# Kernel optimization log

Hardware: AMD Instinct MI355X
Metric: run time of the kernel (lower is better)

## Reference

```python
import jax, jax.numpy as jnp
import numpy as np

PASSES = 6
S = 2           # numEdgeSets
D = 256         # inputLayerSize
OUT = 10        # outputLayerSize
HID = 80
B, N, E = 4, 10000, 160000


def _leaky(x):
    return jax.nn.leaky_relu(x, negative_slope=0.01)


def setup_inputs() -> dict:
    key = jax.random.key(0)
    ks = jax.random.split(key, 18)
    sc = 0.05
    return {
        "nodes": jax.random.normal(ks[0], (B, N, D), jnp.float32),
        "edges": jax.random.randint(ks[1], (B, S, E, 2), 0, N, jnp.int32),
        "problem_type": jax.random.uniform(ks[2], (B, 1), jnp.float32),
        # GRUCell params (torch layout: [3D, D] for ih and hh)
        "gru_w_ih": jax.random.normal(ks[3], (3 * D, D), jnp.float32) * sc,
        "gru_w_hh": jax.random.normal(ks[4], (3 * D, D), jnp.float32) * sc,
        "gru_b_ih": jax.random.normal(ks[5], (3 * D,), jnp.float32) * sc,
        "gru_b_hh": jax.random.normal(ks[6], (3 * D,), jnp.float32) * sc,
        # per-edge-set 2-layer MLP, stacked over edge sets
        "edge_w1": jax.random.normal(ks[7], (S, D, D), jnp.float32) * sc,
        "edge_b1": jax.random.normal(ks[8], (S, D), jnp.float32) * sc,
        "edge_w2": jax.random.normal(ks[9], (S, D, D), jnp.float32) * sc,
        "edge_b2": jax.random.normal(ks[10], (S, D), jnp.float32) * sc,
        # readout head
        "fc1_w": jax.random.normal(ks[11], (HID, D + 1), jnp.float32) * sc,
        "fc1_b": jax.random.normal(ks[12], (HID,), jnp.float32) * sc,
        "fc2_w": jax.random.normal(ks[13], (HID, HID), jnp.float32) * sc,
        "fc2_b": jax.random.normal(ks[14], (HID,), jnp.float32) * sc,
        "fc3_w": jax.random.normal(ks[15], (OUT, HID), jnp.float32) * sc,
        "fc3_b": jax.random.normal(ks[16], (OUT,), jnp.float32) * sc,
    }


def _gru_cell(x, h, w_ih, w_hh, b_ih, b_hh):
    # torch.nn.GRUCell semantics; x,h: [B,N,D]
    gi = jnp.einsum("bnd,ed->bne", x, w_ih) + b_ih   # [B,N,3D]
    gh = jnp.einsum("bnd,ed->bne", h, w_hh) + b_hh
    i_r, i_z, i_n = jnp.split(gi, 3, axis=-1)
    h_r, h_z, h_n = jnp.split(gh, 3, axis=-1)
    r = jax.nn.sigmoid(i_r + h_r)
    z = jax.nn.sigmoid(i_z + h_z)
    n = jnp.tanh(i_n + r * h_n)
    return (1.0 - z) * n + z * h


def reference(nodes, edges, problem_type, gru_w_ih, gru_w_hh, gru_b_ih, gru_b_hh,
              edge_w1, edge_b1, edge_w2, edge_b2,
              fc1_w, fc1_b, fc2_w, fc2_b, fc3_w, fc3_b):
    bidx = jnp.arange(B)[:, None]  # [B,1] for batched scatter
    h = nodes
    for j in range(PASSES):
        incoming = jnp.zeros_like(h)
        for si in range(S):
            dst = edges[:, si, :, 0]  # [B,E]
            src = edges[:, si, :, 1]  # [B,E]
            gathered = jnp.take_along_axis(h, src[:, :, None], axis=1)  # [B,E,D]
            y = _leaky(jnp.einsum("bed,fd->bef", gathered, edge_w1[si]) + edge_b1[si])
            y = jnp.einsum("bed,fd->bef", y, edge_w2[si]) + edge_b2[si]
            incoming = incoming.at[bidx, dst].add(y)
        h = _gru_cell(incoming, h, gru_w_ih, gru_w_hh, gru_b_ih, gru_b_hh)
        if j < PASSES - 2:
            h = jax.lax.stop_gradient(h)  # mirrors .detach()
    # graph readout: sum over nodes, log, nan->0, relu, +inf->finite max
    s = jnp.sum(h, axis=1)               # [B,D]
    l = jnp.log(s)
    l = jnp.where(jnp.isnan(l), 0.0, l)
    l = jax.nn.relu(l)
    finite_max = jnp.max(jnp.where(jnp.isinf(l), -jnp.inf, l), axis=1, keepdims=True)
    l = jnp.where(jnp.isinf(l), finite_max, l)
    x = jnp.concatenate([l, problem_type], axis=1)  # [B,D+1]
    x = _leaky(x @ fc1_w.T + fc1_b)
    x = _leaky(x @ fc2_w.T + fc2_b)
    return x @ fc3_w.T + fc3_b  # [B,OUT]
```

## Files before the change

### kernel.cpp

```cpp
#include <hip/hip_runtime.h>
#include <math.h>

#define NNODES 10000
#define NEDGES 160000
#define DIM    256
#define BATCH  4
#define NG     8
#define MROWS  40064
#define RBLK128 313
#define RGRP128 40

typedef __attribute__((ext_vector_type(8))) __bf16 bf16x8;
typedef __attribute__((ext_vector_type(4))) float  floatx4;
typedef __attribute__((ext_vector_type(8))) unsigned short ushort8v;

__device__ __forceinline__ float leakyf(float x){ return x > 0.f ? x : 0.01f*x; }
__device__ __forceinline__ float fsig(float x){ return 1.f/(1.f + __expf(-x)); }
__device__ __forceinline__ float ftanh(float x){ return 1.f - 2.f/(1.f + __expf(2.f*x)); }
__device__ __forceinline__ unsigned short f2bf_u(float x){
  unsigned int u = __float_as_uint(x);
  u += 0x7fffu + ((u >> 16) & 1u);
  return (unsigned short)(u >> 16);
}
__device__ __forceinline__ float bfdec(unsigned short u){
  return __uint_as_float(((unsigned int)u) << 16);
}
#define GATE_SCL 65535.f
#define GATE_INV 1.5259021896696422e-5f

#define VMCNT8 asm volatile("s_waitcnt vmcnt(8)" ::: "memory")
#define VMCNT4 asm volatile("s_waitcnt vmcnt(4)" ::: "memory")
#define VMCNT0 asm volatile("s_waitcnt vmcnt(0)" ::: "memory")
#define LGKM0  asm volatile("s_waitcnt lgkmcnt(0)" ::: "memory")
#define SBAR   __builtin_amdgcn_s_barrier()
#define SCHEDB __builtin_amdgcn_sched_barrier(0)
#define PRIO1  __builtin_amdgcn_s_setprio(1)
#define PRIO0  __builtin_amdgcn_s_setprio(0)

__device__ __forceinline__ void glds16(unsigned short* lds, const unsigned short* g){
  __builtin_amdgcn_global_load_lds(
      (const __attribute__((address_space(1))) void*)g,
      (__attribute__((address_space(3))) void*)lds, 16, 0, 0);
}

__device__ __forceinline__ ushort8v gload16(const unsigned short* p){
  ushort8v r;
  asm volatile("global_load_dwordx4 %0, %1, off" : "=&v"(r) : "v"(p));
  return r;
}

__global__ void ihinit_kernel(const float* __restrict__ nodes,
                              unsigned short* __restrict__ ihcat,
                              unsigned short* __restrict__ h_lo){
  int idx = blockIdx.x*256 + threadIdx.x;
  int base = idx*4;
  int row = base >> 8, d = base & 255;
  float4 v = *(const float4*)&nodes[base];
  unsigned short h0=f2bf_u(v.x), h1=f2bf_u(v.y), h2=f2bf_u(v.z), h3=f2bf_u(v.w);
  ushort4 hi; hi.x=h0; hi.y=h1; hi.z=h2; hi.w=h3;
  *(ushort4*)&ihcat[(size_t)row*512 + 256 + d] = hi;
  ushort4 lo;
  lo.x = f2bf_u(v.x - bfdec(h0));
  lo.y = f2bf_u(v.y - bfdec(h1));
  lo.z = f2bf_u(v.z - bfdec(h2));
  lo.w = f2bf_u(v.w - bfdec(h3));
  *(ushort4*)&h_lo[base] = lo;
}

__global__ void w1cat_kernel(const float* __restrict__ ew1, unsigned short* __restrict__ o){
  int idx = blockIdx.x*256 + threadIdx.x;
  int n = idx >> 8, k = idx & 255;
  o[idx] = f2bf_u(ew1[(n>>8)*65536 + (n&255)*256 + k]);
}
__global__ void w2k_kernel(const float* __restrict__ ew2, unsigned short* __restrict__ o){
  int idx = blockIdx.x*256 + threadIdx.x;
  int n = idx >> 10, kp = idx & 1023;
  int j = kp & 511, term = kp >> 9;
  int si = j >> 8, k = j & 255;
  float v = ew2[si*65536 + n*256 + k];
  unsigned short h = f2bf_u(v);
  o[idx] = term ? f2bf_u(v - bfdec(h)) : h;
}
__global__ void wk2_kernel(const float* __restrict__ w, unsigned short* __restrict__ o){
  int idx = blockIdx.x*256 + threadIdx.x;
  int c = idx >> 9, kp = idx & 511;
  int k = kp & 255, term = kp >> 8;
  float v = w[c*256 + k];
  unsigned short h = f2bf_u(v);
  o[idx] = term ? f2bf_u(v - bfdec(h)) : h;
}
__global__ void wcomb_kernel(const float* __restrict__ wih, const float* __restrict__ whh,
                             unsigned short* __restrict__ o){
  int idx = blockIdx.x*256 + threadIdx.x;
  int c = idx >> 10, kp = idx & 1023;
  int seg = kp >> 8, k = kp & 255;
  const float* w = (seg & 1) ? whh : wih;
  float v = w[c*256 + k];
  unsigned short h = f2bf_u(v);
  o[idx] = (seg >> 1) ? f2bf_u(v - bfdec(h)) : h;
}

__global__ void hist_kernel(const int* __restrict__ edges, int* __restrict__ cnt){
  int bid = blockIdx.x;
  int g = bid & 7, chunk = bid >> 3;
  int e = chunk*256 + threadIdx.x;
  int d = edges[((size_t)g*NEDGES + e)*2];
  atomicAdd(&cnt[g*NNODES + d], 1);
}

__global__ __launch_bounds__(256) void scanA_kernel(const int* __restrict__ cnt,
                                                    int* __restrict__ off,
                                                    int* __restrict__ tsum){
  __shared__ int sc[256];
  int bid = blockIdx.x;
  int g = bid & 7, c = bid >> 3;
  int t = threadIdx.x;
  int i = c*256 + t;
  int v = (i < NNODES) ? cnt[g*NNODES + i] : 0;
  sc[t] = v;
  __syncthreads();
  for (int o=1;o<256;o<<=1){
    int u = (t>=o) ? sc[t-o] : 0;
    __syncthreads();
    sc[t] += u;
    __syncthreads();
  }
  if (i < NNODES) off[g*(NNODES+1) + i] = sc[t] - v;
  if (t == 255) tsum[g*40 + c] = sc[255];
}
__global__ __launch_bounds__(256) void scanC_kernel(const int* __restrict__ tsum,
                                                    int* __restrict__ off){
  __shared__ int ts[40];
  int bid = blockIdx.x;
  int g = bid & 7, c = bid >> 3;
  int t = threadIdx.x;
  if (t < 40) ts[t] = tsum[g*40 + t];
  __syncthreads();
  int base = 0;
  for (int k=0;k<40;k++) base += (k < c) ? ts[k] : 0;
  int i = c*256 + t;
  if (i < NNODES) off[g*(NNODES+1) + i] += base;
  if (c == 39 && t == 0){
    int tot = 0;
    for (int k=0;k<40;k++) tot += ts[k];
    off[g*(NNODES+1) + NNODES] = tot;
  }
}

__global__ void scatter_kernel(const int* __restrict__ edges, const int* __restrict__ off,
                               int* __restrict__ cur, int* __restrict__ ssrc){
  int bid = blockIdx.x;
  int g = bid & 7, chunk = bid >> 3;
  int e = chunk*256 + threadIdx.x;
  const int* ep = &edges[((size_t)g*NEDGES + e)*2];
  int d = ep[0], s = ep[1];
  int pos = off[g*(NNODES+1) + d] + atomicAdd(&cur[g*NNODES + d], 1);
  ssrc[g*NEDGES + pos] = s;
}

template<int KP, int RS, int KM>
__device__ __forceinline__ void mm128_core(
    const unsigned short* __restrict__ Ab, const unsigned short* __restrict__ Wb,
    unsigned short* lds, floatx4 (&acc)[4][2])
{
  const int t = threadIdx.x;
  const int w = t >> 6, lane = t & 63;
  const int q = lane >> 4, col = lane & 15;
  const int wr = (w >> 2) * 64;
  const int wc = (w & 3) * 32;
  const int sr = t >> 3;
  const int sk = ((t & 7) ^ (sr & 7)) * 8;

  auto STAGE = [&](int kb, int buf){
    unsigned short* Al = lds + buf*16384;
    unsigned short* Bl = Al + 8192;
    #pragma unroll
    for (int i=0;i<2;i++){
      int r = i*64 + sr;
      glds16(&Al[i*4096 + w*512], &Ab[(size_t)r*RS + ((kb + sk) & KM)]);
      glds16(&Bl[i*4096 + w*512], &Wb[(size_t)r*KP + kb + sk]);
    }
  };

  STAGE(0, 0);
  int cur = 0;
  #pragma unroll
  for (int kb = 0; kb < KP; kb += 64){
    if (kb + 64 < KP){
      STAGE(kb + 64, cur^1);
      VMCNT4;
    } else {
      VMCNT0;
    }
    SBAR; SCHEDB;
    const unsigned short* Al = lds + cur*16384;
    const unsigned short* Bl = Al + 8192;
    #pragma unroll
    for (int ks2=0; ks2<2; ks2++){
      bf16x8 a[4], bf[2];
      #pragma unroll
      for (int mi=0;mi<4;mi++){
        int r = wr + mi*16 + col;
        int j = (ks2*4 + q) ^ (r & 7);
        a[mi] = *(const bf16x8*)&Al[r*64 + j*8];
      }
      #pragma unroll
      for (int ni=0;ni<2;ni++){
        int r = wc + ni*16 + col;
        int j = (ks2*4 + q) ^ (r & 7);
        bf[ni] = *(const bf16x8*)&Bl[r*64 + j*8];
      }
      PRIO1;
      #pragma unroll
      for (int mi=0;mi<4;mi++)
        #pragma unroll
        for (int ni=0;ni<2;ni++)
          acc[mi][ni] = __builtin_amdgcn_mfma_f32_16x16x32_bf16(a[mi], bf[ni], acc[mi][ni], 0,0,0);
      PRIO0;
    }
    SCHEDB; LGKM0; SBAR;
    cur ^= 1;
  }
}

__device__ __forceinline__ void mm128x2_core(
    const unsigned short* __restrict__ A1, const unsigned short* __restrict__ W1,
    const unsigned short* __restrict__ A2, const unsigned short* __restrict__ W2,
    unsigned short* lds, floatx4 (&ai)[4][2], floatx4 (&ah)[4][2])
{
  const int t = threadIdx.x;
  const int w = t >> 6, lane = t & 63;
  const int q = lane >> 4, col = lane & 15;
  const int wr = (w >> 2) * 64;
  const int wc = (w & 3) * 32;
  const int sr = t >> 3;
  const int sk = ((t & 7) ^ (sr & 7)) * 8;

  auto STAGE = [&](int s, int buf){
    const unsigned short* A = (s < 8) ? A1 : A2;
    const unsigned short* W = (s < 8) ? W1 : W2;
    int kb = (s & 7) * 64;
    unsigned short* Al = lds + buf*16384;
    unsigned short* Bl = Al + 8192;
    #pragma unroll
    for (int i=0;i<2;i++){
      int r = i*64 + sr;
      glds16(&Al[i*4096 + w*512], &A[(size_t)r*512 + ((kb + sk) & 255)]);
      glds16(&Bl[i*4096 + w*512], &W[(size_t)r*512 + kb + sk]);
    }
  };

  STAGE(0, 0);
  int cur = 0;
  #pragma unroll
  for (int s = 0; s < 16; s++){
    if (s < 15){
      STAGE(s + 1, cur^1);
      VMCNT4;
    } else {
      VMCNT0;
    }
    SBAR; SCHEDB;
    const unsigned short* Al = lds + cur*16384;
    const unsigned short* Bl = Al + 8192;
    #pragma unroll
    for (int ks2=0; ks2<2; ks2++){
      bf16x8 a[4], bf[2];
      #pragma unroll
      for (int mi=0;mi<4;mi++){
        int r = wr + mi*16 + col;
        int j = (ks2*4 + q) ^ (r & 7);
        a[mi] = *(const bf16x8*)&Al[r*64 + j*8];
      }
      #pragma unroll
      for (int ni=0;ni<2;ni++){
        int r = wc + ni*16 + col;
        int j = (ks2*4 + q) ^ (r & 7);
        bf[ni] = *(const bf16x8*)&Bl[r*64 + j*8];
      }
      PRIO1;
      if (s < 8){
        #pragma unroll
        for (int mi=0;mi<4;mi++)
          #pragma unroll
          for (int ni=0;ni<2;ni++)
            ai[mi][ni] = __builtin_amdgcn_mfma_f32_16x16x32_bf16(a[mi], bf[ni], ai[mi][ni], 0,0,0);
      } else {
        #pragma unroll
        for (int mi=0;mi<4;mi++)
          #pragma unroll
          for (int ni=0;ni<2;ni++)
            ah[mi][ni] = __builtin_amdgcn_mfma_f32_16x16x32_bf16(a[mi], bf[ni], ah[mi][ni], 0,0,0);
      }
      PRIO0;
    }
    SCHEDB; LGKM0; SBAR;
    cur ^= 1;
  }
}

#define XDECODE128(NCOL) \
  const int bid_ = blockIdx.x; \
  const int rb_ = ((bid_ >> 3) / NCOL) * 8 + (bid_ & 7); \
  const int colb_ = (bid_ >> 3) % NCOL; \
  if (rb_ >= RBLK128) return;

#define MMPRO128 \
  const int t = threadIdx.x, w = t >> 6, lane = t & 63; \
  const int q = lane >> 4, col = lane & 15; \
  const int wrq = (w >> 2) * 64, wcq = (w & 3) * 32; \
  floatx4 acc[4][2]; \
  _Pragma("unroll") for (int mi=0;mi<4;mi++) _Pragma("unroll") for (int ni=0;ni<2;ni++) \
    acc[mi][ni] = (floatx4){0.f,0.f,0.f,0.f};

__global__ __launch_bounds__(512,4) void z64_kernel(
    const unsigned short* __restrict__ ihcat, const unsigned short* __restrict__ w1cat,
    const float* __restrict__ eb1, unsigned short* __restrict__ Z)
{
  __shared__ unsigned short lds[32768];
  XDECODE128(4)
  const int row0 = rb_*128, col0 = colb_*128;
  MMPRO128
  mm128_core<256,512,255>(ihcat + (size_t)row0*512 + 256, w1cat + (size_t)col0*256, lds, acc);

  #pragma unroll
  for (int ni=0;ni<2;ni++){
    int n = col0 + wcq + ni*16 + col;
    int si = n >> 8, cz = n & 255;
    float bb = eb1[si*256 + cz];
    unsigned short* zp = Z + (size_t)si*MROWS*256 + cz;
    #pragma unroll
    for (int mi=0;mi<4;mi++)
      #pragma unroll
      for (int rr=0;rr<4;rr++){
        int row = row0 + wrq + mi*16 + q*4 + rr;
        zp[(size_t)row*256] = f2bf_u(leakyf(acc[mi][ni][rr] + bb));
      }
  }
}

#define ACC4(B) do { \
  a0 += bfdec(u[B][0])+bfdec(u[B+1][0])+bfdec(u[B+2][0])+bfdec(u[B+3][0]); \
  a1 += bfdec(u[B][1])+bfdec(u[B+1][1])+bfdec(u[B+2][1])+bfdec(u[B+3][1]); \
  a2 += bfdec(u[B][2])+bfdec(u[B+1][2])+bfdec(u[B+2][2])+bfdec(u[B+3][2]); \
  a3 += bfdec(u[B][3])+bfdec(u[B+1][3])+bfdec(u[B+2][3])+bfdec(u[B+3][3]); \
  a4 += bfdec(u[B][4])+bfdec(u[B+1][4])+bfdec(u[B+2][4])+bfdec(u[B+3][4]); \
  a5 += bfdec(u[B][5])+bfdec(u[B+1][5])+bfdec(u[B+2][5])+bfdec(u[B+3][5]); \
  a6 += bfdec(u[B][6])+bfdec(u[B+1][6])+bfdec(u[B+2][6])+bfdec(u[B+3][6]); \
  a7 += bfdec(u[B][7])+bfdec(u[B+1][7])+bfdec(u[B+2][7])+bfdec(u[B+3][7]); \
} while(0)

__global__ __launch_bounds__(256,2) void aggregate_kernel(
    const unsigned short* __restrict__ Z, const int* __restrict__ ssrc,
    const int* __restrict__ off, unsigned short* __restrict__ Sb)
{
  const int bid = blockIdx.x;
  const int g = bid & 7;
  const int dgrp = bid >> 3;
  const int b = g >> 1, si = g & 1;
  const int w = threadIdx.x >> 6, lane = threadIdx.x & 63;
  const int half = lane >> 5, c = lane & 31;
  const unsigned short* zb = Z + ((size_t)si*MROWS + b*10000)*256 + c*8;
  const int* sp = ssrc + (size_t)g*NEDGES;
  const int* offg = off + g*(NNODES+1);

  #pragma unroll
  for (int p=0;p<2;p++){
    const int d = dgrp*16 + w*4 + p*2 + half;
    int j = offg[d];
    const int j1 = offg[d+1];
    float a0=0.f,a1=0.f,a2=0.f,a3=0.f,a4=0.f,a5=0.f,a6=0.f,a7=0.f;
    for (; j+16 <= j1; j+=16){
      int s[16];
      #pragma unroll
      for (int e=0;e<16;e++) s[e] = sp[j+e];
      ushort8v u[16];
      #pragma unroll
      for (int e=0;e<16;e++) u[e] = gload16(zb + (size_t)s[e]*256);
      VMCNT8; SCHEDB;
      ACC4(0); ACC4(4);
      VMCNT0; SCHEDB;
      ACC4(8); ACC4(12);
    }
    if (j+8 <= j1){
      int s[8];
      #pragma unroll
      for (int e=0;e<8;e++) s[e] = sp[j+e];
      ushort8v u[8];
      #pragma unroll
      for (int e=0;e<8;e++) u[e] = gload16(zb + (size_t)s[e]*256);
      VMCNT0; SCHEDB;
      ACC4(0); ACC4(4);
      j += 8;
    }
    if (j+4 <= j1){
      int s[4];
      #pragma unroll
      for (int e=0;e<4;e++) s[e] = sp[j+e];
      ushort8v u[4];
      #pragma unroll
      for (int e=0;e<4;e++) u[e] = gload16(zb + (size_t)s[e]*256);
      VMCNT0; SCHEDB;
      ACC4(0);
      j += 4;
    }
    for (; j < j1; j++){
      ushort8v uu = *(const ushort8v*)&zb[(size_t)sp[j]*256];
      a0+=bfdec(uu[0]); a1+=bfdec(uu[1]); a2+=bfdec(uu[2]); a3+=bfdec(uu[3]);
      a4+=bfdec(uu[4]); a5+=bfdec(uu[5]); a6+=bfdec(uu[6]); a7+=bfdec(uu[7]);
    }
    size_t so = (size_t)(b*10000 + d)*512 + si*256 + c*8;
    ushort8v hv;
    hv[0]=f2bf_u(a0); hv[1]=f2bf_u(a1); hv[2]=f2bf_u(a2); hv[3]=f2bf_u(a3);
    hv[4]=f2bf_u(a4); hv[5]=f2bf_u(a5); hv[6]=f2bf_u(a6); hv[7]=f2bf_u(a7);
    *(ushort8v*)&Sb[so] = hv;
  }
}

__global__ __launch_bounds__(512,4) void w264_kernel(
    const unsigned short* __restrict__ Sb, const unsigned short* __restrict__ w2k,
    const float* __restrict__ eb2, const int* __restrict__ off,
    unsigned short* __restrict__ ihcat)
{
  __shared__ unsigned short lds[32768];
  XDECODE128(2)
  const int row0 = rb_*128, col0 = colb_*128;
  MMPRO128
  mm128_core<1024,512,511>(Sb + (size_t)row0*512, w2k + (size_t)col0*1024, lds, acc);

  float b20[2], b21[2];
  #pragma unroll
  for (int ni=0;ni<2;ni++){
    int n = col0 + wcq + ni*16 + col;
    b20[ni] = eb2[n];
    b21[ni] = eb2[256 + n];
  }
  #pragma unroll
  for (int mi=0;mi<4;mi++)
    #pragma unroll
    for (int rr=0;rr<4;rr++){
      int row = row0 + wrq + mi*16 + q*4 + rr;
      int rw = (row < 40000) ? row : 39999;
      int b = rw / 10000, d = rw - b*10000;
      int o0 = (b*2)*(NNODES+1) + d;
      int o1 = (b*2+1)*(NNODES+1) + d;
      float dg0 = (float)(off[o0+1] - off[o0]);
      float dg1 = (float)(off[o1+1] - off[o1]);
      #pragma unroll
      for (int ni=0;ni<2;ni++){
        int n = col0 + wcq + ni*16 + col;
        ihcat[(size_t)row*512 + n] = f2bf_u(acc[mi][ni][rr] + dg0*b20[ni] + dg1*b21[ni]);
      }
    }
}

__global__ __launch_bounds__(512,4) void gruA_kernel(
    const unsigned short* __restrict__ ihcat, const unsigned short* __restrict__ wcomb,
    const float* __restrict__ b_ih, const float* __restrict__ b_hh,
    unsigned short* __restrict__ rz_r, unsigned short* __restrict__ rz_z)
{
  __shared__ unsigned short lds[32768];
  XDECODE128(4)
  const int row0 = rb_*128, col0 = colb_*128;
  MMPRO128
  mm128_core<1024,512,511>(ihcat + (size_t)row0*512, wcomb + (size_t)col0*1024, lds, acc);

  float bb[2];
  #pragma unroll
  for (int ni=0;ni<2;ni++){
    int n = col0 + wcq + ni*16 + col;
    bb[ni] = b_ih[n] + b_hh[n];
  }
  unsigned short* dst = (col0 < 256) ? rz_r : rz_z;
  const int cbase = (col0 & 255) + wcq;
  #pragma unroll
  for (int mi=0;mi<4;mi++)
    #pragma unroll
    for (int rr=0;rr<4;rr++){
      size_t row = (size_t)(row0 + wrq + mi*16 + q*4 + rr);
      #pragma unroll
      for (int ni=0;ni<2;ni++){
        float v = fsig(acc[mi][ni][rr] + bb[ni]);
        dst[row*256 + cbase + ni*16 + col] = (unsigned short)(v*GATE_SCL + 0.5f);
      }
    }
}

__global__ __launch_bounds__(512,2) void gruB_kernel(
    const unsigned short* __restrict__ ihcat, unsigned short* __restrict__ h_lo,
    const unsigned short* __restrict__ wihk, const unsigned short* __restrict__ whhk,
    const float* __restrict__ b_ih, const float* __restrict__ b_hh,
    const unsigned short* __restrict__ rz_r, const unsigned short* __restrict__ rz_z,
    unsigned short* __restrict__ ihcat_nxt)
{
  __shared__ unsigned short lds[32768];
  XDECODE128(2)
  const int row0 = rb_*128, dcol0 = colb_*128;
  const int t = threadIdx.x, w = t >> 6, lane = t & 63;
  const int q = lane >> 4, col = lane & 15;
  const int wrq = (w >> 2) * 64, wcq = (w & 3) * 32;

  floatx4 ai[4][2], ah[4][2];
  #pragma unroll
  for (int mi=0;mi<4;mi++)
    #pragma unroll
    for (int ni=0;ni<2;ni++){ ai[mi][ni] = (floatx4){0.f,0.f,0.f,0.f}; ah[mi][ni] = (floatx4){0.f,0.f,0.f,0.f}; }

  mm128x2_core(ihcat + (size_t)row0*512,       wihk + (size_t)(512 + dcol0)*512,
               ihcat + (size_t)row0*512 + 256, whhk + (size_t)(512 + dcol0)*512,
               lds, ai, ah);

  float bi[2], bh[2];
  #pragma unroll
  for (int ni=0;ni<2;ni++){
    int n = 512 + dcol0 + wcq + ni*16 + col;
    bi[ni] = b_ih[n]; bh[ni] = b_hh[n];
  }
  #pragma unroll
  for (int mi=0;mi<4;mi++)
    #pragma unroll
    for (int rr=0;rr<4;rr++){
      size_t row = (size_t)(row0 + wrq + mi*16 + q*4 + rr);
      #pragma unroll
      for (int ni=0;ni<2;ni++){
        int dn = dcol0 + wcq + ni*16 + col;
        float rg = (float)rz_r[row*256 + dn] * GATE_INV;
        float zg = (float)rz_z[row*256 + dn] * GATE_INV;
        float ng = ftanh(ai[mi][ni][rr] + bi[ni] + rg*(ah[mi][ni][rr] + bh[ni]));
        float hv = bfdec(ihcat[row*512 + 256 + dn]) + bfdec(h_lo[row*256 + dn]);
        float hnew = (1.f - zg)*ng + zg*hv;
        unsigned short hh = f2bf_u(hnew);
        ihcat_nxt[row*512 + 256 + dn] = hh;
        h_lo[row*256 + dn] = f2bf_u(hnew - bfdec(hh));
      }
    }
}

__global__ void reduce_kernel(const unsigned short* __restrict__ ihcat,
                              const unsigned short* __restrict__ h_lo,
                              float* __restrict__ sbuf){
  int b  = blockIdx.x / 50;
  int s0 = (blockIdx.x % 50) * 200;
  int d  = threadIdx.x;
  size_t row = (size_t)b*NNODES + s0;
  float acc = 0.f;
  for (int i=0;i<200;i++){
    acc += bfdec(ihcat[(row+i)*512 + 256 + d]) + bfdec(h_lo[(row+i)*256 + d]);
  }
  atomicAdd(&sbuf[b*DIM + d], acc);
}

__global__ __launch_bounds__(320) void head_kernel(
    const float* __restrict__ sbuf, const float* __restrict__ pt,
    const float* __restrict__ fc1w, const float* __restrict__ fc1b,
    const float* __restrict__ fc2w, const float* __restrict__ fc2b,
    const float* __restrict__ fc3w, const float* __restrict__ fc3b,
    float* __restrict__ out)
{
  __shared__ float L[4][257];
  __shared__ float T1[4][80];
  __shared__ float T2[4][80];
  __shared__ float fmx[4];
  int t = threadIdx.x;
  if (t < 256){
    for (int b=0;b<4;b++){
      float v = sbuf[b*DIM + t];
      float ll = logf(v);
      if (ll != ll) ll = 0.f;
      ll = fmaxf(ll, 0.f);
      L[b][t] = ll;
    }
  }
  __syncthreads();
  int w = t >> 6, lane = t & 63;
  if (w < 4){
    float m = -INFINITY;
    for (int i=lane;i<256;i+=64){ float v = L[w][i]; if (v != INFINITY) m = fmaxf(m, v); }
    #pragma unroll
    for (int o=32;o>=1;o>>=1) m = fmaxf(m, __shfl_xor(m, o, 64));
    if (lane==0) fmx[w] = m;
  }
  __syncthreads();
  if (t < 256){
    for (int b=0;b<4;b++) if (L[b][t] == INFINITY) L[b][t] = fmx[b];
  }
  if (t < 4) L[t][256] = pt[t];
  __syncthreads();
  if (t < 320){
    int b = t/80, i = t%80;
    float a = fc1b[i];
    for (int k=0;k<257;k++) a += L[b][k]*fc1w[i*257+k];
    T1[b][i] = leakyf(a);
  }
  __syncthreads();
  if (t < 320){
    int b = t/80, i = t%80;
    float a = fc2b[i];
    for (int k=0;k<80;k++) a += T1[b][k]*fc2w[i*80+k];
    T2[b][i] = leakyf(a);
  }
  __syncthreads();
  if (t < 40){
    int b = t/10, i = t%10;
    float a = fc3b[i];
    for (int k=0;k<80;k++) a += T2[b][k]*fc3w[i*80+k];
    out[b*10+i] = a;
  }
}

extern "C" void kernel_launch(void* const* d_in, const int* in_sizes, int n_in,
                              void* d_out, int out_size, void* d_ws, size_t ws_size,
                              hipStream_t stream) {
  const float* nodes = (const float*)d_in[0];
  const int*   edges = (const int*)d_in[1];
  const float* pt    = (const float*)d_in[2];
  const float* w_ih  = (const float*)d_in[3];
  const float* w_hh  = (const float*)d_in[4];
  const float* b_ih  = (const float*)d_in[5];
  const float* b_hh  = (const float*)d_in[6];
  const float* ew1   = (const float*)d_in[7];
  const float* eb1   = (const float*)d_in[8];
  const float* ew2   = (const float*)d_in[9];
  const float* eb2   = (const float*)d_in[10];
  const float* fc1w  = (const float*)d_in[11];
  const float* fc1b  = (const float*)d_in[12];
  const float* fc2w  = (const float*)d_in[13];
  const float* fc2b  = (const float*)d_in[14];
  const float* fc3w  = (const float*)d_in[15];
  const float* fc3b  = (const float*)d_in[16];

  const size_t HN  = (size_t)BATCH*NNODES*DIM;
  const size_t HNP = (size_t)MROWS*DIM;
  char* p = (char*)d_ws;
  float* sbuf = (float*)p;                        p += BATCH*DIM*4;
  unsigned short* ihcat0 = (unsigned short*)p;    p += (size_t)MROWS*512*2;
  unsigned short* ihcat1 = (unsigned short*)p;    p += (size_t)MROWS*512*2;
  unsigned short* h_lo   = (unsigned short*)p;    p += HNP*2;
  unsigned short* Zb   = (unsigned short*)p;      p += 2*HNP*2;
  unsigned short* Sb   = (unsigned short*)p;      p += (size_t)MROWS*512*2;
  unsigned short* w1cat= (unsigned short*)p;      p += 512*256*2;
  unsigned short* w2k  = (unsigned short*)p;      p += 256*1024*2;
  unsigned short* wihk = (unsigned short*)p;      p += 768*512*2;
  unsigned short* whhk = (unsigned short*)p;      p += 768*512*2;
  unsigned short* wcomb= (unsigned short*)p;      p += 512*1024*2;
  int* off  = (int*)p;                            p += NG*(NNODES+1)*4;
  int* cur  = (int*)p;                            p += NG*NNODES*4;
  int* ssrc = (int*)p;                            p += (size_t)NG*NEDGES*4;

  unsigned short* rz_r = (unsigned short*)Sb;
  unsigned short* rz_z = rz_r + (size_t)MROWS*256;
  int* tsum = (int*)sbuf;

  w1cat_kernel<<<512,256,0,stream>>>(ew1, w1cat);
  w2k_kernel<<<1024,256,0,stream>>>(ew2, w2k);
  wk2_kernel<<<1536,256,0,stream>>>(w_ih, wihk);
  wk2_kernel<<<1536,256,0,stream>>>(w_hh, whhk);
  wcomb_kernel<<<2048,256,0,stream>>>(w_ih, w_hh, wcomb);

  ihinit_kernel<<<(int)(HN/1024),256,0,stream>>>(nodes, ihcat0, h_lo);

  hipMemsetAsync(cur, 0, NG*NNODES*sizeof(int), stream);
  hist_kernel<<<(NG*NEDGES)/256,256,0,stream>>>(edges, cur);
  scanA_kernel<<<NG*40,256,0,stream>>>(cur, off, tsum);
  scanC_kernel<<<NG*40,256,0,stream>>>(tsum, off);
  hipMemsetAsync(cur, 0, NG*NNODES*sizeof(int), stream);
  scatter_kernel<<<(NG*NEDGES)/256,256,0,stream>>>(edges, off, cur, ssrc);

  hipMemsetAsync(sbuf, 0, BATCH*DIM*sizeof(float), stream);

  unsigned short* ih[2] = {ihcat0, ihcat1};

  for (int pass=0; pass<6; pass++){
    unsigned short* curb = ih[pass & 1];
    unsigned short* nxtb = ih[(pass+1) & 1];
    z64_kernel<<<RGRP128*8*4,512,0,stream>>>(curb, w1cat, eb1, Zb);
    aggregate_kernel<<<5000,256,0,stream>>>(Zb, ssrc, off, Sb);
    w264_kernel<<<RGRP128*8*2,512,0,stream>>>(Sb, w2k, eb2, off, curb);
    gruA_kernel<<<RGRP128*8*4,512,0,stream>>>(curb, wcomb, b_ih, b_hh, rz_r, rz_z);
    gruB_kernel<<<RGRP128*8*2,512,0,stream>>>(curb, h_lo, wihk, whhk, b_ih, b_hh,
                                              rz_r, rz_z, nxtb);
  }
  reduce_kernel<<<200,256,0,stream>>>(ih[0], h_lo, sbuf);
  head_kernel<<<1,320,0,stream>>>(sbuf, pt, fc1w,fc1b,fc2w,fc2b,fc3w,fc3b,(float*)d_out);
}
```

Baseline: 1.487 ms.

## Fuse GRU gate kernels into one kernel computing r, z, n in registers

Merges gruA (r/z gate GEMM plus sigmoid written to a global buffer) and gruB (n-gate GEMMs plus update) into one kernel. Each block now runs a 48-stage pipelined K loop that accumulates four sets of accumulators (r, z, ih_n, hh_n), so the r/z gates never round-trip through global memory and one launch is removed. The cost is doubled accumulator register pressure (64 floatx4 per thread) under launch_bounds(512,2), which may cause spills or lower occupancy. The grid is also halved relative to gruA, so there is less parallelism per launch.

```diff
diff --git a/kernel.cpp b/kernel.cpp
--- a/kernel.cpp
+++ b/kernel.cpp
@@ -223,38 +223,52 @@
   }
 }
 
-__device__ __forceinline__ void mm128x2_core(
-    const unsigned short* __restrict__ A1, const unsigned short* __restrict__ W1,
-    const unsigned short* __restrict__ A2, const unsigned short* __restrict__ W2,
-    unsigned short* lds, floatx4 (&ai)[4][2], floatx4 (&ah)[4][2])
+__device__ __forceinline__ void mmgru_core(
+    const unsigned short* __restrict__ Arow, const unsigned short* __restrict__ Wr,
+    const unsigned short* __restrict__ Wz,   const unsigned short* __restrict__ Wi,
+    const unsigned short* __restrict__ Wh,
+    unsigned short* lds,
+    floatx4 (&ar)[4][2], floatx4 (&az)[4][2],
+    floatx4 (&ai)[4][2], floatx4 (&ah)[4][2])
 {
   const int t = threadIdx.x;
   const int w = t >> 6, lane = t & 63;
   const int q = lane >> 4, col = lane & 15;
-  const int wr = (w >> 2) * 64;
-  const int wc = (w & 3) * 32;
+  const int wr_ = (w >> 2) * 64;
+  const int wc_ = (w & 3) * 32;
   const int sr = t >> 3;
   const int sk = ((t & 7) ^ (sr & 7)) * 8;
 
   auto STAGE = [&](int s, int buf){
-    const unsigned short* A = (s < 8) ? A1 : A2;
-    const unsigned short* W = (s < 8) ? W1 : W2;
-    int kb = (s & 7) * 64;
     unsigned short* Al = lds + buf*16384;
     unsigned short* Bl = Al + 8192;
-    #pragma unroll
-    for (int i=0;i<2;i++){
-      int r = i*64 + sr;
-      glds16(&Al[i*4096 + w*512], &A[(size_t)r*512 + ((kb + sk) & 255)]);
-      glds16(&Bl[i*4096 + w*512], &W[(size_t)r*512 + kb + sk]);
+    if (s < 32){
+      int kb = (s & 15) * 64;
+      const unsigned short* W = (s < 16) ? Wr : Wz;
+      #pragma unroll
+      for (int i=0;i<2;i++){
+        int r = i*64 + sr;
+        glds16(&Al[i*4096 + w*512], &Arow[(size_t)r*512 + ((kb + sk) & 511)]);
+        glds16(&Bl[i*4096 + w*512], &W[(size_t)r*1024 + kb + sk]);
+      }
+    } else {
+      int kb = (s & 7) * 64;
+      const unsigned short* A = (s < 40) ? Arow : (Arow + 256);
+      const unsigned short* W = (s < 40) ? Wi : Wh;
+      #pragma unroll
+      for (int i=0;i<2;i++){
+        int r = i*64 + sr;
+        glds16(&Al[i*4096 + w*512], &A[(size_t)r*512 + ((kb + sk) & 255)]);
+        glds16(&Bl[i*4096 + w*512], &W[(size_t)r*512 + kb + sk]);
+      }
     }
   };
 
   STAGE(0, 0);
   int cur = 0;
   #pragma unroll
-  for (int s = 0; s < 16; s++){
-    if (s < 15){
+  for (int s = 0; s < 48; s++){
+    if (s < 47){
       STAGE(s + 1, cur^1);
       VMCNT4;
     } else {
@@ -268,18 +282,30 @@
       bf16x8 a[4], bf[2];
       #pragma unroll
       for (int mi=0;mi<4;mi++){
-        int r = wr + mi*16 + col;
+        int r = wr_ + mi*16 + col;
         int j = (ks2*4 + q) ^ (r & 7);
         a[mi] = *(const bf16x8*)&Al[r*64 + j*8];
       }
       #pragma unroll
       for (int ni=0;ni<2;ni++){
-        int r = wc + ni*16 + col;
+        int r = wc_ + ni*16 + col;
         int j = (ks2*4 + q) ^ (r & 7);
         bf[ni] = *(const bf16x8*)&Bl[r*64 + j*8];
       }
       PRIO1;
-      if (s < 8){
+      if (s < 16){
+        #pragma unroll
+        for (int mi=0;mi<4;mi++)
+          #pragma unroll
+          for (int ni=0;ni<2;ni++)
+            ar[mi][ni] = __builtin_amdgcn_mfma_f32_16x16x32_bf16(a[mi], bf[ni], ar[mi][ni], 0,0,0);
+      } else if (s < 32){
+        #pragma unroll
+        for (int mi=0;mi<4;mi++)
+          #pragma unroll
+          for (int ni=0;ni<2;ni++)
+            az[mi][ni] = __builtin_amdgcn_mfma_f32_16x16x32_bf16(a[mi], bf[ni], az[mi][ni], 0,0,0);
+      } else if (s < 40){
         #pragma unroll
         for (int mi=0;mi<4;mi++)
           #pragma unroll
@@ -454,43 +480,11 @@
     }
 }
 
-__global__ __launch_bounds__(512,4) void gruA_kernel(
-    const unsigned short* __restrict__ ihcat, const unsigned short* __restrict__ wcomb,
-    const float* __restrict__ b_ih, const float* __restrict__ b_hh,
-    unsigned short* __restrict__ rz_r, unsigned short* __restrict__ rz_z)
-{
-  __shared__ unsigned short lds[32768];
-  XDECODE128(4)
-  const int row0 = rb_*128, col0 = colb_*128;
-  MMPRO128
-  mm128_core<1024,512,511>(ihcat + (size_t)row0*512, wcomb + (size_t)col0*1024, lds, acc);
-
-  float bb[2];
-  #pragma unroll
-  for (int ni=0;ni<2;ni++){
-    int n = col0 + wcq + ni*16 + col;
-    bb[ni] = b_ih[n] + b_hh[n];
-  }
-  unsigned short* dst = (col0 < 256) ? rz_r : rz_z;
-  const int cbase = (col0 & 255) + wcq;
-  #pragma unroll
-  for (int mi=0;mi<4;mi++)
-    #pragma unroll
-    for (int rr=0;rr<4;rr++){
-      size_t row = (size_t)(row0 + wrq + mi*16 + q*4 + rr);
-      #pragma unroll
-      for (int ni=0;ni<2;ni++){
-        float v = fsig(acc[mi][ni][rr] + bb[ni]);
-        dst[row*256 + cbase + ni*16 + col] = (unsigned short)(v*GATE_SCL + 0.5f);
-      }
-    }
-}
-
-__global__ __launch_bounds__(512,2) void gruB_kernel(
+__global__ __launch_bounds__(512,2) void gru_kernel(
     const unsigned short* __restrict__ ihcat, unsigned short* __restrict__ h_lo,
+    const unsigned short* __restrict__ wcomb,
     const unsigned short* __restrict__ wihk, const unsigned short* __restrict__ whhk,
     const float* __restrict__ b_ih, const float* __restrict__ b_hh,
-    const unsigned short* __restrict__ rz_r, const unsigned short* __restrict__ rz_z,
     unsigned short* __restrict__ ihcat_nxt)
 {
   __shared__ unsigned short lds[32768];
@@ -500,21 +494,32 @@
   const int q = lane >> 4, col = lane & 15;
   const int wrq = (w >> 2) * 64, wcq = (w & 3) * 32;
 
-  floatx4 ai[4][2], ah[4][2];
+  floatx4 ar[4][2], az[4][2], ai[4][2], ah[4][2];
   #pragma unroll
   for (int mi=0;mi<4;mi++)
     #pragma unroll
-    for (int ni=0;ni<2;ni++){ ai[mi][ni] = (floatx4){0.f,0.f,0.f,0.f}; ah[mi][ni] = (floatx4){0.f,0.f,0.f,0.f}; }
-
-  mm128x2_core(ihcat + (size_t)row0*512,       wihk + (size_t)(512 + dcol0)*512,
-               ihcat + (size_t)row0*512 + 256, whhk + (size_t)(512 + dcol0)*512,
-               lds, ai, ah);
-
-  float bi[2], bh[2];
+    for (int ni=0;ni<2;ni++){
+      ar[mi][ni] = (floatx4){0.f,0.f,0.f,0.f};
+      az[mi][ni] = (floatx4){0.f,0.f,0.f,0.f};
+      ai[mi][ni] = (floatx4){0.f,0.f,0.f,0.f};
+      ah[mi][ni] = (floatx4){0.f,0.f,0.f,0.f};
+    }
+
+  mmgru_core(ihcat + (size_t)row0*512,
+             wcomb + (size_t)dcol0*1024,
+             wcomb + (size_t)(256 + dcol0)*1024,
+             wihk  + (size_t)(512 + dcol0)*512,
+             whhk  + (size_t)(512 + dcol0)*512,
+             lds, ar, az, ai, ah);
+
+  float br[2], bz[2], bi[2], bh[2];
   #pragma unroll
   for (int ni=0;ni<2;ni++){
-    int n = 512 + dcol0 + wcq + ni*16 + col;
-    bi[ni] = b_ih[n]; bh[ni] = b_hh[n];
+    int dn = dcol0 + wcq + ni*16 + col;
+    br[ni] = b_ih[dn]       + b_hh[dn];
+    bz[ni] = b_ih[256 + dn] + b_hh[256 + dn];
+    bi[ni] = b_ih[512 + dn];
+    bh[ni] = b_hh[512 + dn];
   }
   #pragma unroll
   for (int mi=0;mi<4;mi++)
@@ -524,8 +529,12 @@
       #pragma unroll
       for (int ni=0;ni<2;ni++){
         int dn = dcol0 + wcq + ni*16 + col;
-        float rg = (float)rz_r[row*256 + dn] * GATE_INV;
-        float zg = (float)rz_z[row*256 + dn] * GATE_INV;
+        float rv = fsig(ar[mi][ni][rr] + br[ni]);
+        float zv = fsig(az[mi][ni][rr] + bz[ni]);
+        unsigned short rq = (unsigned short)(rv*GATE_SCL + 0.5f);
+        unsigned short zq = (unsigned short)(zv*GATE_SCL + 0.5f);
+        float rg = (float)rq * GATE_INV;
+        float zg = (float)zq * GATE_INV;
         float ng = ftanh(ai[mi][ni][rr] + bi[ni] + rg*(ah[mi][ni][rr] + bh[ni]));
         float hv = bfdec(ihcat[row*512 + 256 + dn]) + bfdec(h_lo[row*256 + dn]);
         float hnew = (1.f - zg)*ng + zg*hv;
@@ -647,8 +656,6 @@
   int* cur  = (int*)p;                            p += NG*NNODES*4;
   int* ssrc = (int*)p;                            p += (size_t)NG*NEDGES*4;
 
-  unsigned short* rz_r = (unsigned short*)Sb;
-  unsigned short* rz_z = rz_r + (size_t)MROWS*256;
   int* tsum = (int*)sbuf;
 
   w1cat_kernel<<<512,256,0,stream>>>(ew1, w1cat);
@@ -676,9 +683,8 @@
     z64_kernel<<<RGRP128*8*4,512,0,stream>>>(curb, w1cat, eb1, Zb);
     aggregate_kernel<<<5000,256,0,stream>>>(Zb, ssrc, off, Sb);
     w264_kernel<<<RGRP128*8*2,512,0,stream>>>(Sb, w2k, eb2, off, curb);
-    gruA_kernel<<<RGRP128*8*4,512,0,stream>>>(curb, wcomb, b_ih, b_hh, rz_r, rz_z);
-    gruB_kernel<<<RGRP128*8*2,512,0,stream>>>(curb, h_lo, wihk, whhk, b_ih, b_hh,
-                                              rz_r, rz_z, nxtb);
+    gru_kernel<<<RGRP128*8*2,512,0,stream>>>(curb, h_lo, wcomb, wihk, whhk,
+                                             b_ih, b_hh, nxtb);
   }
   reduce_kernel<<<200,256,0,stream>>>(ih[0], h_lo, sbuf);
   head_kernel<<<1,320,0,stream>>>(sbuf, pt, fc1w,fc1b,fc2w,fc2b,fc3w,fc3b,(float*)d_out);
```

New measurement: 1.622 ms. +9.1%, slower.
